# Kernel optimization log

Measured on AMD Instinct MI355X. Metric: run time of the kernel, lower is better.

## Reference

```python
import jax, jax.numpy as jnp
import numpy as np

B, S, H, NH, HD, FF, E, K = 2, 1024, 1024, 16, 64, 4096, 8, 2
EPS = 1e-6
ROPE_BASE = 10000.0


def setup_inputs() -> dict:
    key = jax.random.key(0)
    ks = jax.random.split(key, 10)
    std = 0.02
    return {
        "hidden_states": jax.random.normal(ks[0], (B, S, H), jnp.float32),
        "attention_mask": jnp.zeros((1, 1, S, S), jnp.float32),
        "ln1_w": jnp.ones((H,), jnp.float32),
        "ln2_w": jnp.ones((H,), jnp.float32),
        "Wq": jax.random.normal(ks[1], (H, H), jnp.float32) * std,
        "Wk": jax.random.normal(ks[2], (H, H), jnp.float32) * std,
        "Wv": jax.random.normal(ks[3], (H, H), jnp.float32) * std,
        "Wo": jax.random.normal(ks[4], (H, H), jnp.float32) * std,
        "Wr": jax.random.normal(ks[5], (E, H), jnp.float32) * std,
        "Wg": jax.random.normal(ks[6], (E, FF, H), jnp.float32) * std,
        "Wu": jax.random.normal(ks[7], (E, FF, H), jnp.float32) * std,
        "Wd": jax.random.normal(ks[8], (E, H, FF), jnp.float32) * std,
    }


def _rmsnorm(x, w):
    rms = jnp.sqrt(jnp.mean(x * x, axis=-1, keepdims=True) + EPS)
    return x / rms * w


def _rotate_half(x):
    x1, x2 = x[..., : x.shape[-1] // 2], x[..., x.shape[-1] // 2:]
    return jnp.concatenate((-x2, x1), axis=-1)


def _forward(hidden_states, attention_mask, ln1_w, ln2_w, Wq, Wk, Wv, Wo, Wr, Wg, Wu, Wd):
    residual = hidden_states
    x = _rmsnorm(hidden_states, ln1_w)

    # attention projections -> [B, NH, S, HD]
    def split_heads(t):
        return t.reshape(B, S, NH, HD).transpose(0, 2, 1, 3)

    q = split_heads(x @ Wq.T)
    k = split_heads(x @ Wk.T)
    v = split_heads(x @ Wv.T)

    # RoPE
    inv_freq = 1.0 / (ROPE_BASE ** (jnp.arange(0, HD, 2, dtype=jnp.float32) / HD))
    freqs = jnp.outer(jnp.arange(S, dtype=jnp.float32), inv_freq)  # [S, HD/2]
    emb = jnp.concatenate((freqs, freqs), axis=-1)  # [S, HD]
    cos = jnp.cos(emb)[None, None]
    sin = jnp.sin(emb)[None, None]
    q = q * cos + _rotate_half(q) * sin
    k = k * cos + _rotate_half(k) * sin

    scale = HD ** -0.5
    scores = jnp.einsum("bhqd,bhkd->bhqk", q, k) * scale + attention_mask
    attn = jax.nn.softmax(scores.astype(jnp.float32), axis=-1).astype(q.dtype)
    out = jnp.einsum("bhqk,bhkd->bhqd", attn, v)
    out = out.transpose(0, 2, 1, 3).reshape(B, S, H) @ Wo.T

    hidden = residual + out  # dropout is identity in eval

    # MoE FFN
    residual2 = hidden
    x2 = _rmsnorm(hidden, ln2_w)
    router_logits = x2 @ Wr.T  # [B, S, E]
    router_probs = jax.nn.softmax(router_logits, axis=-1)
    expert_weights, expert_indices = jax.lax.top_k(router_probs, K)  # [B,S,K]
    expert_weights = expert_weights / jnp.sum(expert_weights, axis=-1, keepdims=True)

    # load-balance loss
    num_tokens = B * S
    counts = jnp.sum(expert_indices[..., None] == jnp.arange(E), axis=(0, 1, 2)).astype(jnp.float32)
    expert_usage = counts / num_tokens  # [E]
    mean_routing_prob = router_probs.mean(axis=(0, 1))  # [E]
    lb_loss = jnp.sum(expert_usage * mean_routing_prob) * E

    moe_out = jnp.zeros_like(x2)
    for e in range(E):
        # combine weight is 0 for tokens not routed to expert e -> same math as masked gather/scatter
        w_e = jnp.sum(expert_weights * (expert_indices == e), axis=-1, keepdims=True)  # [B,S,1]
        y = (jax.nn.silu(x2 @ Wg[e].T) * (x2 @ Wu[e].T)) @ Wd[e].T
        moe_out = moe_out + w_e * y

    hidden = residual2 + moe_out
    return hidden, lb_loss


def reference(hidden_states, attention_mask, ln1_w, ln2_w, Wq, Wk, Wv, Wo, Wr, Wg, Wu, Wd):
    return _forward(hidden_states, attention_mask, ln1_w, ln2_w, Wq, Wk, Wv, Wo, Wr, Wg, Wu, Wd)
```

## Files before the change

### kernel.cpp

```cpp
#include <hip/hip_runtime.h>
#include <cstdint>
#include <cstddef>

#define DI __device__ __forceinline__

namespace {

constexpr int B_ = 2, S_ = 1024, H_ = 1024, NH_ = 16, FF_ = 4096, E_ = 8;
constexpr int T_ = B_ * S_;
constexpr int MAXTILES = (T_ * 2) / 128 + E_;
constexpr int PADSLOTS = MAXTILES * 128;
constexpr size_t APL = (size_t)T_ * H_;
constexpr size_t WPL = (size_t)H_ * H_;

typedef __attribute__((ext_vector_type(8))) short short8;
typedef __attribute__((ext_vector_type(4))) float f32x4;

DI float bf2f(unsigned short u) { return __uint_as_float(((unsigned)u) << 16); }
DI unsigned short f2bf(float f) {
  unsigned u = __float_as_uint(f);
  u += 0x7fffu + ((u >> 16) & 1u);
  return (unsigned short)(u >> 16);
}
DI void cvt8(const float4 a, const float4 b, unsigned short* d) {
  d[0] = f2bf(a.x); d[1] = f2bf(a.y); d[2] = f2bf(a.z); d[3] = f2bf(a.w);
  d[4] = f2bf(b.x); d[5] = f2bf(b.y); d[6] = f2bf(b.z); d[7] = f2bf(b.w);
}

template <int MODE>
__global__ __launch_bounds__(256) void rmsnorm_kernel(const float* __restrict__ in,
                                                      const float* __restrict__ w,
                                                      float* __restrict__ out,
                                                      unsigned short* __restrict__ outb) {
  const int t = blockIdx.x, tid = threadIdx.x;
  const float4* row = (const float4*)(in + (size_t)t * H_);
  float4 v = row[tid];
  float ss = v.x * v.x + v.y * v.y + v.z * v.z + v.w * v.w;
  #pragma unroll
  for (int off = 32; off; off >>= 1) ss += __shfl_down(ss, off);
  __shared__ float red[4];
  if ((tid & 63) == 0) red[tid >> 6] = ss;
  __syncthreads();
  const float total = red[0] + red[1] + red[2] + red[3];
  const float rinv = 1.f / sqrtf(total * (1.f / (float)H_) + 1e-6f);
  const float4 wv = ((const float4*)w)[tid];
  float o[4];
  o[0] = v.x * rinv * wv.x; o[1] = v.y * rinv * wv.y;
  o[2] = v.z * rinv * wv.z; o[3] = v.w * rinv * wv.w;
  if (MODE == 1) {
    float4 o4 = {o[0], o[1], o[2], o[3]};
    ((float4*)(out + (size_t)t * H_))[tid] = o4;
    unsigned short* p = outb + (size_t)t * H_ + tid * 4;
    p[0] = f2bf(o[0]); p[1] = f2bf(o[1]); p[2] = f2bf(o[2]); p[3] = f2bf(o[3]);
  } else {
    __align__(8) unsigned short hi[4], lo[4];
    #pragma unroll
    for (int j = 0; j < 4; j++) {
      hi[j] = f2bf(o[j]);
      lo[j] = f2bf(o[j] - bf2f(hi[j]));
    }
    const size_t idx = (size_t)t * H_ + tid * 4;
    *(uint2*)&outb[idx] = *(const uint2*)hi;
    *(uint2*)&outb[APL + idx] = *(const uint2*)lo;
  }
}

__global__ __launch_bounds__(256) void cvt_wsplit(const float* __restrict__ src,
                                                  unsigned short* __restrict__ dst, int n8) {
  const int i = blockIdx.x * 256 + threadIdx.x;
  if (i < n8) {
    const float4 a = ((const float4*)src)[2 * i];
    const float4 b = ((const float4*)src)[2 * i + 1];
    const float xs[8] = {a.x, a.y, a.z, a.w, b.x, b.y, b.z, b.w};
    __align__(16) unsigned short hi[8], lo[8];
    #pragma unroll
    for (int j = 0; j < 8; j++) {
      hi[j] = f2bf(xs[j]);
      lo[j] = f2bf(xs[j] - bf2f(hi[j]));
    }
    ((uint4*)dst)[i] = *(const uint4*)hi;
    ((uint4*)(dst + WPL))[i] = *(const uint4*)lo;
  }
}

__global__ __launch_bounds__(256) void cvt_ws(const float* __restrict__ src,
                                              unsigned short* __restrict__ dst, int n8) {
  const int i = blockIdx.x * 256 + threadIdx.x;
  if (i < n8) {
    const float4 a = ((const float4*)src)[2 * i];
    const float4 b = ((const float4*)src)[2 * i + 1];
    __align__(16) unsigned short t[8];
    cvt8(a, b, t);
    ((uint4*)dst)[i] = *(const uint4*)t;
  }
}

template <int EPI>
__global__ __launch_bounds__(256, 3) void gemm_split(const unsigned short* __restrict__ As,
                                                     const unsigned short* __restrict__ Wsa,
                                                     const unsigned short* __restrict__ Wsb,
                                                     const unsigned short* __restrict__ Wsc,
                                                     float* __restrict__ Ca,
                                                     float* __restrict__ Cb,
                                                     float* __restrict__ Cc,
                                                     const float* __restrict__ resid) {
  constexpr int K = 1024;
  constexpr int LDA = 40;
  __shared__ __align__(16) unsigned short sAh[128 * LDA];
  __shared__ __align__(16) unsigned short sAl[128 * LDA];
  __shared__ __align__(16) unsigned short sWh[128 * LDA];
  __shared__ __align__(16) unsigned short sWl[128 * LDA];
  const int tid = threadIdx.x;
  const int m0 = blockIdx.x << 7, n0 = blockIdx.y << 7;
  const unsigned short* W = Wsa; float* C = Ca;
  if (EPI == 0) {
    if (blockIdx.z == 1) { W = Wsb; C = Cb; }
    else if (blockIdx.z == 2) { W = Wsc; C = Cc; }
  }
  const int wave = tid >> 6, lane = tid & 63, wm = wave >> 1, wn = wave & 1;
  const int g16 = lane >> 4, l15 = lane & 15;
  const int row = tid >> 1, kq = (tid & 1) << 4;
  const unsigned short* pah = As + (size_t)(m0 + row) * K + kq;
  const unsigned short* pal = pah + APL;
  const unsigned short* pwh = W + (size_t)(n0 + row) * K + kq;
  const unsigned short* pwl = pwh + WPL;
  f32x4 acc[4][4];
  #pragma unroll
  for (int m = 0; m < 4; m++)
    #pragma unroll
    for (int n = 0; n < 4; n++) acc[m][n] = (f32x4){0.f, 0.f, 0.f, 0.f};

  uint4 rah0 = *(const uint4*)pah, rah1 = *(const uint4*)(pah + 8);
  uint4 ral0 = *(const uint4*)pal, ral1 = *(const uint4*)(pal + 8);
  uint4 rwh0 = *(const uint4*)pwh, rwh1 = *(const uint4*)(pwh + 8);
  uint4 rwl0 = *(const uint4*)pwl, rwl1 = *(const uint4*)(pwl + 8);

  for (int k0 = 0; k0 < K; k0 += 32) {
    __syncthreads();
    *(uint4*)&sAh[row * LDA + kq] = rah0;
    *(uint4*)&sAh[row * LDA + kq + 8] = rah1;
    *(uint4*)&sAl[row * LDA + kq] = ral0;
    *(uint4*)&sAl[row * LDA + kq + 8] = ral1;
    *(uint4*)&sWh[row * LDA + kq] = rwh0;
    *(uint4*)&sWh[row * LDA + kq + 8] = rwh1;
    *(uint4*)&sWl[row * LDA + kq] = rwl0;
    *(uint4*)&sWl[row * LDA + kq + 8] = rwl1;
    if (k0 + 32 < K) {
      rah0 = *(const uint4*)(pah + k0 + 32); rah1 = *(const uint4*)(pah + k0 + 40);
      ral0 = *(const uint4*)(pal + k0 + 32); ral1 = *(const uint4*)(pal + k0 + 40);
      rwh0 = *(const uint4*)(pwh + k0 + 32); rwh1 = *(const uint4*)(pwh + k0 + 40);
      rwl0 = *(const uint4*)(pwl + k0 + 32); rwl1 = *(const uint4*)(pwl + k0 + 40);
    }
    __syncthreads();
    short8 ah[4], al[4], wh[4], wl[4];
    #pragma unroll
    for (int m = 0; m < 4; m++) {
      ah[m] = *(const short8*)&sAh[(wm * 64 + m * 16 + l15) * LDA + g16 * 8];
      al[m] = *(const short8*)&sAl[(wm * 64 + m * 16 + l15) * LDA + g16 * 8];
    }
    #pragma unroll
    for (int n = 0; n < 4; n++) {
      wh[n] = *(const short8*)&sWh[(wn * 64 + n * 16 + l15) * LDA + g16 * 8];
      wl[n] = *(const short8*)&sWl[(wn * 64 + n * 16 + l15) * LDA + g16 * 8];
    }
    #pragma unroll
    for (int m = 0; m < 4; m++)
      #pragma unroll
      for (int n = 0; n < 4; n++) {
        acc[m][n] = __builtin_amdgcn_mfma_f32_16x16x32_bf16(ah[m], wh[n], acc[m][n], 0, 0, 0);
        acc[m][n] = __builtin_amdgcn_mfma_f32_16x16x32_bf16(al[m], wh[n], acc[m][n], 0, 0, 0);
        acc[m][n] = __builtin_amdgcn_mfma_f32_16x16x32_bf16(ah[m], wl[n], acc[m][n], 0, 0, 0);
      }
  }
  #pragma unroll
  for (int m = 0; m < 4; m++)
    #pragma unroll
    for (int r = 0; r < 4; r++) {
      const int grow = m0 + wm * 64 + m * 16 + g16 * 4 + r;
      #pragma unroll
      for (int n = 0; n < 4; n++) {
        const int gcol = n0 + wn * 64 + n * 16 + l15;
        float v = acc[m][n][r];
        if (EPI == 1) v += resid[(size_t)grow * 1024 + gcol];
        C[(size_t)grow * 1024 + gcol] = v;
      }
    }
}

__global__ __launch_bounds__(256) void rope_kernel(float* __restrict__ buf) {
  const int id = blockIdx.x * 256 + threadIdx.x;
  const int t = id >> 9;
  const int rem = id & 511;
  const int h = rem >> 5, j = rem & 31;
  const int s = t & (S_ - 1);
  const float inv = exp2f(-(float)j * (0.41524101186092029f));
  const float ang = (float)s * inv;
  const float c = cosf(ang), sn = sinf(ang);
  float* p = buf + (size_t)t * H_ + h * 64;
  const float xa = p[j], xb = p[j + 32];
  p[j] = xa * c - xb * sn;
  p[j + 32] = xb * c + xa * sn;
}

__global__ __launch_bounds__(512, 2) void attn_mfma(const float* __restrict__ q,
                                                    const float* __restrict__ k,
                                                    const float* __restrict__ v,
                                                    unsigned short* __restrict__ aos) {
  constexpr int LDW = 136;
  __shared__ __align__(16) unsigned short sP[128 * LDW];
  __shared__ __align__(16) unsigned short sK[64 * LDW];
  __shared__ __align__(16) unsigned short sVt[64 * LDW];
  const int tid = threadIdx.x;
  const int bh = blockIdx.x >> 3, chunk = blockIdx.x & 7;
  const int b = bh >> 4, h = bh & (NH_ - 1);
  const int w = tid >> 6, lane = tid & 63, g = lane >> 4, l15 = lane & 15;

  {
    const int row = tid >> 2, d0 = (tid & 3) << 4;
    const float* qp = q + ((size_t)((b << 10) + (chunk << 7) + row)) * H_ + h * 64 + d0;
    __align__(16) unsigned short thi[16], tlo[16];
    #pragma unroll
    for (int c = 0; c < 4; c++) {
      const float4 x = ((const float4*)qp)[c];
      const float xs[4] = {x.x, x.y, x.z, x.w};
      #pragma unroll
      for (int j = 0; j < 4; j++) {
        const float val = xs[j] * 0.125f;
        const unsigned short hi = f2bf(val);
        thi[c * 4 + j] = hi;
        tlo[c * 4 + j] = f2bf(val - bf2f(hi));
      }
    }
    uint4* dh = (uint4*)&sP[row * LDW + d0];
    dh[0] = ((const uint4*)thi)[0]; dh[1] = ((const uint4*)thi)[1];
    uint4* dl = (uint4*)&sP[row * LDW + 64 + d0];
    dl[0] = ((const uint4*)tlo)[0]; dl[1] = ((const uint4*)tlo)[1];
  }
  __syncthreads();
  short8 aqh[2], aql[2];
  #pragma unroll
  for (int s2 = 0; s2 < 2; s2++) {
    aqh[s2] = *(const short8*)&sP[(w * 16 + l15) * LDW + s2 * 32 + g * 8];
    aql[s2] = *(const short8*)&sP[(w * 16 + l15) * LDW + 64 + s2 * 32 + g * 8];
  }
  __syncthreads();

  f32x4 accO[4];
  #pragma unroll
  for (int n = 0; n < 4; n++) accO[n] = (f32x4){0.f, 0.f, 0.f, 0.f};
  float mrun[4] = {-3.0e38f, -3.0e38f, -3.0e38f, -3.0e38f};
  float lrun[4] = {0.f, 0.f, 0.f, 0.f};

  const int krow = tid >> 3, dk0 = (tid & 7) << 3;
  const int vd = tid >> 3, vk0 = (tid & 7) << 3;
  const float* kp0 = k + ((size_t)((b << 10) + krow)) * H_ + h * 64 + dk0;
  const float* vp0 = v + ((size_t)(b << 10)) * H_ + h * 64 + vd;

  float krg[8], vrg[8];
  {
    const float4 a = *(const float4*)kp0;
    const float4 c = *(const float4*)(kp0 + 4);
    krg[0] = a.x; krg[1] = a.y; krg[2] = a.z; krg[3] = a.w;
    krg[4] = c.x; krg[5] = c.y; krg[6] = c.z; krg[7] = c.w;
    #pragma unroll
    for (int i = 0; i < 8; i++) vrg[i] = vp0[(size_t)(vk0 + i) * H_];
  }
  {
    __align__(16) unsigned short thi[8], tlo[8];
    #pragma unroll
    for (int j = 0; j < 8; j++) {
      const unsigned short hi = f2bf(krg[j]);
      thi[j] = hi; tlo[j] = f2bf(krg[j] - bf2f(hi));
    }
    *(uint4*)&sK[krow * LDW + dk0] = *(const uint4*)thi;
    *(uint4*)&sK[krow * LDW + 64 + dk0] = *(const uint4*)tlo;
    #pragma unroll
    for (int j = 0; j < 8; j++) {
      const unsigned short hi = f2bf(vrg[j]);
      thi[j] = hi; tlo[j] = f2bf(vrg[j] - bf2f(hi));
    }
    *(uint4*)&sVt[vd * LDW + vk0] = *(const uint4*)thi;
    *(uint4*)&sVt[vd * LDW + 64 + vk0] = *(const uint4*)tlo;
  }
  __syncthreads();

  for (int kt = 0; kt < S_ / 64; kt++) {
    if (kt < S_ / 64 - 1) {
      const float* kp = kp0 + (size_t)((kt + 1) * 64) * H_;
      const float4 a = *(const float4*)kp;
      const float4 c = *(const float4*)(kp + 4);
      krg[0] = a.x; krg[1] = a.y; krg[2] = a.z; krg[3] = a.w;
      krg[4] = c.x; krg[5] = c.y; krg[6] = c.z; krg[7] = c.w;
      #pragma unroll
      for (int i = 0; i < 8; i++) vrg[i] = vp0[(size_t)((kt + 1) * 64 + vk0 + i) * H_];
    }
    f32x4 accS[4];
    #pragma unroll
    for (int n = 0; n < 4; n++) accS[n] = (f32x4){0.f, 0.f, 0.f, 0.f};
    #pragma unroll
    for (int s2 = 0; s2 < 2; s2++) {
      #pragma unroll
      for (int n = 0; n < 4; n++) {
        const short8 bkh = *(const short8*)&sK[(n * 16 + l15) * LDW + s2 * 32 + g * 8];
        const short8 bkl = *(const short8*)&sK[(n * 16 + l15) * LDW + 64 + s2 * 32 + g * 8];
        accS[n] = __builtin_amdgcn_mfma_f32_16x16x32_bf16(aqh[s2], bkh, accS[n], 0, 0, 0);
        accS[n] = __builtin_amdgcn_mfma_f32_16x16x32_bf16(aql[s2], bkh, accS[n], 0, 0, 0);
        accS[n] = __builtin_amdgcn_mfma_f32_16x16x32_bf16(aqh[s2], bkl, accS[n], 0, 0, 0);
      }
    }
    float corr[4];
    float pv_[4][4];
    #pragma unroll
    for (int r = 0; r < 4; r++) {
      float tm = fmaxf(fmaxf(accS[0][r], accS[1][r]), fmaxf(accS[2][r], accS[3][r]));
      tm = fmaxf(tm, __shfl_xor(tm, 1));
      tm = fmaxf(tm, __shfl_xor(tm, 2));
      tm = fmaxf(tm, __shfl_xor(tm, 4));
      tm = fmaxf(tm, __shfl_xor(tm, 8));
      const float mnew = fmaxf(mrun[r], tm);
      corr[r] = __expf(mrun[r] - mnew);
      mrun[r] = mnew;
      float ssum = 0.f;
      #pragma unroll
      for (int n = 0; n < 4; n++) {
        const float p = __expf(accS[n][r] - mnew);
        pv_[n][r] = p; ssum += p;
      }
      ssum += __shfl_xor(ssum, 1);
      ssum += __shfl_xor(ssum, 2);
      ssum += __shfl_xor(ssum, 4);
      ssum += __shfl_xor(ssum, 8);
      lrun[r] = lrun[r] * corr[r] + ssum;
    }
    #pragma unroll
    for (int n = 0; n < 4; n++)
      #pragma unroll
      for (int r = 0; r < 4; r++) accO[n][r] *= corr[r];
    #pragma unroll
    for (int n = 0; n < 4; n++)
      #pragma unroll
      for (int r = 0; r < 4; r++) {
        const float p = pv_[n][r];
        const unsigned short hi = f2bf(p);
        unsigned short* pp = &sP[(w * 16 + g * 4 + r) * LDW + (n * 16 + l15)];
        pp[0] = hi;
        pp[64] = f2bf(p - bf2f(hi));
      }
    #pragma unroll
    for (int s2 = 0; s2 < 2; s2++) {
      const short8 aph = *(const short8*)&sP[(w * 16 + l15) * LDW + s2 * 32 + g * 8];
      const short8 apl = *(const short8*)&sP[(w * 16 + l15) * LDW + 64 + s2 * 32 + g * 8];
      #pragma unroll
      for (int n = 0; n < 4; n++) {
        const short8 bvh = *(const short8*)&sVt[(n * 16 + l15) * LDW + s2 * 32 + g * 8];
        const short8 bvl = *(const short8*)&sVt[(n * 16 + l15) * LDW + 64 + s2 * 32 + g * 8];
        accO[n] = __builtin_amdgcn_mfma_f32_16x16x32_bf16(aph, bvh, accO[n], 0, 0, 0);
        accO[n] = __builtin_amdgcn_mfma_f32_16x16x32_bf16(apl, bvh, accO[n], 0, 0, 0);
        accO[n] = __builtin_amdgcn_mfma_f32_16x16x32_bf16(aph, bvl, accO[n], 0, 0, 0);
      }
    }
    __syncthreads();
    if (kt < S_ / 64 - 1) {
      __align__(16) unsigned short thi[8], tlo[8];
      #pragma unroll
      for (int j = 0; j < 8; j++) {
        const unsigned short hi = f2bf(krg[j]);
        thi[j] = hi; tlo[j] = f2bf(krg[j] - bf2f(hi));
      }
      *(uint4*)&sK[krow * LDW + dk0] = *(const uint4*)thi;
      *(uint4*)&sK[krow * LDW + 64 + dk0] = *(const uint4*)tlo;
      #pragma unroll
      for (int j = 0; j < 8; j++) {
        const unsigned short hi = f2bf(vrg[j]);
        thi[j] = hi; tlo[j] = f2bf(vrg[j] - bf2f(hi));
      }
      *(uint4*)&sVt[vd * LDW + vk0] = *(const uint4*)thi;
      *(uint4*)&sVt[vd * LDW + 64 + vk0] = *(const uint4*)tlo;
    }
    __syncthreads();
  }
  float inv[4];
  #pragma unroll
  for (int r = 0; r < 4; r++) inv[r] = 1.f / lrun[r];
  unsigned short* aoh = aos + ((size_t)((b << 10) + (chunk << 7) + w * 16)) * H_ + h * 64;
  #pragma unroll
  for (int n = 0; n < 4; n++)
    #pragma unroll
    for (int r = 0; r < 4; r++) {
      const float val = accO[n][r] * inv[r];
      const unsigned short hi = f2bf(val);
      const size_t idx = (size_t)(g * 4 + r) * H_ + n * 16 + l15;
      aoh[idx] = hi;
      aoh[APL + idx] = f2bf(val - bf2f(hi));
    }
}

__global__ __launch_bounds__(256) void router_kernel(const float* __restrict__ x2,
                                                     const float* __restrict__ Wr,
                                                     float* __restrict__ probs,
                                                     int* __restrict__ texp,
                                                     float* __restrict__ tw) {
  const int wid = threadIdx.x >> 6, lane = threadIdx.x & 63;
  const int t = (blockIdx.x << 2) + wid;
  const float* xr = x2 + (size_t)t * H_;
  float4 xv[4];
  #pragma unroll
  for (int i = 0; i < 4; i++) xv[i] = *(const float4*)&xr[(i << 8) + (lane << 2)];
  float acc[E_];
  #pragma unroll
  for (int e = 0; e < E_; e++) acc[e] = 0.f;
  #pragma unroll
  for (int i = 0; i < 4; i++) {
    #pragma unroll
    for (int e = 0; e < E_; e++) {
      const float4 wv = *(const float4*)&Wr[e * H_ + (i << 8) + (lane << 2)];
      acc[e] += xv[i].x * wv.x + xv[i].y * wv.y + xv[i].z * wv.z + xv[i].w * wv.w;
    }
  }
  #pragma unroll
  for (int e = 0; e < E_; e++) {
    #pragma unroll
    for (int off = 32; off; off >>= 1) acc[e] += __shfl_xor(acc[e], off);
  }
  if (lane == 0) {
    float mx = acc[0];
    #pragma unroll
    for (int e = 1; e < E_; e++) mx = fmaxf(mx, acc[e]);
    float pp[E_]; float sum = 0.f;
    #pragma unroll
    for (int e = 0; e < E_; e++) { pp[e] = __expf(acc[e] - mx); sum += pp[e]; }
    const float isum = 1.f / sum;
    #pragma unroll
    for (int e = 0; e < E_; e++) pp[e] *= isum;
    float4 p0 = {pp[0], pp[1], pp[2], pp[3]};
    float4 p1 = {pp[4], pp[5], pp[6], pp[7]};
    *(float4*)&probs[(size_t)t * E_] = p0;
    *(float4*)&probs[(size_t)t * E_ + 4] = p1;
    int e0 = 0; float b0 = pp[0];
    #pragma unroll
    for (int e = 1; e < E_; e++) if (pp[e] > b0) { b0 = pp[e]; e0 = e; }
    int e1 = -1; float b1 = -1.f;
    #pragma unroll
    for (int e = 0; e < E_; e++) if (e != e0 && pp[e] > b1) { b1 = pp[e]; e1 = e; }
    const float iw = 1.f / (b0 + b1);
    texp[2 * t] = e0; texp[2 * t + 1] = e1;
    tw[2 * t] = b0 * iw; tw[2 * t + 1] = b1 * iw;
  }
}

__global__ __launch_bounds__(256) void fill_slots(int* slot_tok, float* slot_w) {
  const int i = blockIdx.x * 256 + threadIdx.x;
  if (i < PADSLOTS) { slot_tok[i] = -1; slot_w[i] = 0.f; }
}

__global__ __launch_bounds__(256) void finalize_kernel(const float* __restrict__ probs,
                                                       const int* __restrict__ texp,
                                                       const float* __restrict__ tw,
                                                       int* __restrict__ ntiles,
                                                       int* __restrict__ tile_expert,
                                                       int* __restrict__ slot_tok,
                                                       float* __restrict__ slot_w,
                                                       float* __restrict__ lb_out) {
  const int tid = threadIdx.x;
  const int w = tid >> 6, lane = tid & 63;
  __shared__ float sRed[4][E_];
  __shared__ int sCnt[4][E_];
  __shared__ int sPoff[E_];
  __shared__ int sBase[E_];
  __shared__ int sWcnt[4][E_];

  float ps[E_];
  #pragma unroll
  for (int e = 0; e < E_; e++) ps[e] = 0.f;
  #pragma unroll
  for (int i = 0; i < T_ / 256; i++) {
    const float4* pr = (const float4*)&probs[(size_t)(i * 256 + tid) * E_];
    const float4 a = pr[0], b = pr[1];
    ps[0] += a.x; ps[1] += a.y; ps[2] += a.z; ps[3] += a.w;
    ps[4] += b.x; ps[5] += b.y; ps[6] += b.z; ps[7] += b.w;
  }
  #pragma unroll
  for (int e = 0; e < E_; e++) {
    #pragma unroll
    for (int off = 32; off; off >>= 1) ps[e] += __shfl_xor(ps[e], off);
  }
  int cnt[E_];
  #pragma unroll
  for (int e = 0; e < E_; e++) cnt[e] = 0;
  #pragma unroll
  for (int i = 0; i < 2 * T_ / 256; i++) {
    const int ee = texp[i * 256 + tid];
    #pragma unroll
    for (int e = 0; e < E_; e++) cnt[e] += (ee == e) ? 1 : 0;
  }
  #pragma unroll
  for (int e = 0; e < E_; e++) {
    #pragma unroll
    for (int off = 32; off; off >>= 1) cnt[e] += __shfl_xor(cnt[e], off);
  }
  if (lane == 0) {
    #pragma unroll
    for (int e = 0; e < E_; e++) { sRed[w][e] = ps[e]; sCnt[w][e] = cnt[e]; }
  }
  __syncthreads();
  if (tid == 0) {
    int off = 0, tc = 0;
    float lb = 0.f;
    for (int e = 0; e < E_; e++) {
      const int c = sCnt[0][e] + sCnt[1][e] + sCnt[2][e] + sCnt[3][e];
      const float p = sRed[0][e] + sRed[1][e] + sRed[2][e] + sRed[3][e];
      sPoff[e] = off;
      const int nt = (c + 127) >> 7;
      for (int i = 0; i < nt; i++) tile_expert[tc++] = e;
      off += nt << 7;
      lb += ((float)c / (float)T_) * (p / (float)T_);
    }
    *ntiles = tc;
    lb_out[0] = lb * (float)E_;
  }
  if (tid < E_) sBase[tid] = 0;
  __syncthreads();
  for (int c = 0; c < 2 * T_ / 256; c++) {
    const int i = c * 256 + tid;
    const int e = texp[i];
    const float wv = tw[i];
    int myrank = 0;
    #pragma unroll
    for (int ee = 0; ee < E_; ee++) {
      const unsigned long long m = __ballot(e == ee);
      if (lane == 0) sWcnt[w][ee] = (int)__popcll(m);
      if (e == ee) myrank = (int)__popcll(m & ((1ull << lane) - 1ull));
    }
    __syncthreads();
    int pre = 0;
    #pragma unroll
    for (int w2 = 0; w2 < 4; w2++) if (w2 < w) pre += sWcnt[w2][e];
    const int slot = sPoff[e] + sBase[e] + pre + myrank;
    slot_tok[slot] = i >> 1;
    slot_w[slot] = wv;
    __syncthreads();
    if (tid < E_) sBase[tid] += sWcnt[0][tid] + sWcnt[1][tid] + sWcnt[2][tid] + sWcnt[3][tid];
    __syncthreads();
  }
}

__global__ __launch_bounds__(256, 2) void moe_gemm1(const unsigned short* __restrict__ x2b,
                                                    const float* __restrict__ Wg,
                                                    const float* __restrict__ Wu,
                                                    const int* __restrict__ slot_tok,
                                                    const int* __restrict__ tile_expert,
                                                    const int* __restrict__ ntiles,
                                                    unsigned short* __restrict__ hbuf) {
  const int bid = blockIdx.x;
  const int tile = bid >> 6;
  const int n0 = (bid & 63) << 6;
  if (tile >= *ntiles) return;
  constexpr int K = 1024;
  constexpr int LDA = 72;
  __shared__ __align__(16) unsigned short sA[128 * LDA];
  __shared__ __align__(16) unsigned short sG[64 * LDA];
  __shared__ __align__(16) unsigned short sU[64 * LDA];
  __shared__ int stok[128];
  const int tid = threadIdx.x;
  if (tid < 128) stok[tid] = slot_tok[tile * 128 + tid];
  __syncthreads();
  const int e = tile_expert[tile];
  const int wave = tid >> 6, lane = tid & 63, wm = wave >> 1, wn = wave & 1;
  const int g16 = lane >> 4, l15 = lane & 15;
  const int arow = tid >> 2, akq = (tid & 3) << 4;
  const int grow = tid >> 2, gkq = (tid & 3) << 3;
  int tok0 = stok[arow];       if (tok0 < 0) tok0 = 0;
  int tok1 = stok[64 + arow];  if (tok1 < 0) tok1 = 0;
  const unsigned short* a0 = x2b + (size_t)tok0 * K + akq;
  const unsigned short* a1 = x2b + (size_t)tok1 * K + akq;
  const float* gp = Wg + ((size_t)e * FF_ + n0 + grow) * K + gkq;
  const float* up = Wu + ((size_t)e * FF_ + n0 + grow) * K + gkq;

  f32x4 ag[4][2], au[4][2];
  #pragma unroll
  for (int m = 0; m < 4; m++)
    #pragma unroll
    for (int n = 0; n < 2; n++) { ag[m][n] = (f32x4){0,0,0,0}; au[m][n] = (f32x4){0,0,0,0}; }

  uint4 ra0 = *(const uint4*)a0, ra1 = *(const uint4*)(a0 + 8);
  uint4 ra2 = *(const uint4*)a1, ra3 = *(const uint4*)(a1 + 8);
  float4 rg[4], ru[4];
  rg[0] = *(const float4*)gp;        rg[1] = *(const float4*)(gp + 4);
  rg[2] = *(const float4*)(gp + 32); rg[3] = *(const float4*)(gp + 36);
  ru[0] = *(const float4*)up;        ru[1] = *(const float4*)(up + 4);
  ru[2] = *(const float4*)(up + 32); ru[3] = *(const float4*)(up + 36);

  for (int k0 = 0; k0 < K; k0 += 64) {
    __align__(16) unsigned short tg[16], tu[16];
    cvt8(rg[0], rg[1], tg); cvt8(rg[2], rg[3], tg + 8);
    cvt8(ru[0], ru[1], tu); cvt8(ru[2], ru[3], tu + 8);
    __syncthreads();
    *(uint4*)&sA[arow * LDA + akq] = ra0;
    *(uint4*)&sA[arow * LDA + akq + 8] = ra1;
    *(uint4*)&sA[(arow + 64) * LDA + akq] = ra2;
    *(uint4*)&sA[(arow + 64) * LDA + akq + 8] = ra3;
    *(uint4*)&sG[grow * LDA + gkq] = ((const uint4*)tg)[0];
    *(uint4*)&sG[grow * LDA + gkq + 32] = ((const uint4*)tg)[1];
    *(uint4*)&sU[grow * LDA + gkq] = ((const uint4*)tu)[0];
    *(uint4*)&sU[grow * LDA + gkq + 32] = ((const uint4*)tu)[1];
    if (k0 + 64 < K) {
      ra0 = *(const uint4*)(a0 + k0 + 64); ra1 = *(const uint4*)(a0 + k0 + 72);
      ra2 = *(const uint4*)(a1 + k0 + 64); ra3 = *(const uint4*)(a1 + k0 + 72);
      rg[0] = *(const float4*)(gp + k0 + 64); rg[1] = *(const float4*)(gp + k0 + 68);
      rg[2] = *(const float4*)(gp + k0 + 96); rg[3] = *(const float4*)(gp + k0 + 100);
      ru[0] = *(const float4*)(up + k0 + 64); ru[1] = *(const float4*)(up + k0 + 68);
      ru[2] = *(const float4*)(up + k0 + 96); ru[3] = *(const float4*)(up + k0 + 100);
    }
    __syncthreads();
    #pragma unroll
    for (int ks = 0; ks < 2; ks++) {
      const int ko = ks * 32 + g16 * 8;
      short8 af[4], gf[2], uf[2];
      #pragma unroll
      for (int m = 0; m < 4; m++)
        af[m] = *(const short8*)&sA[(wm * 64 + m * 16 + l15) * LDA + ko];
      #pragma unroll
      for (int n = 0; n < 2; n++) {
        gf[n] = *(const short8*)&sG[(wn * 32 + n * 16 + l15) * LDA + ko];
        uf[n] = *(const short8*)&sU[(wn * 32 + n * 16 + l15) * LDA + ko];
      }
      #pragma unroll
      for (int m = 0; m < 4; m++)
        #pragma unroll
        for (int n = 0; n < 2; n++) {
          ag[m][n] = __builtin_amdgcn_mfma_f32_16x16x32_bf16(af[m], gf[n], ag[m][n], 0, 0, 0);
          au[m][n] = __builtin_amdgcn_mfma_f32_16x16x32_bf16(af[m], uf[n], au[m][n], 0, 0, 0);
        }
    }
  }
  #pragma unroll
  for (int m = 0; m < 4; m++)
    #pragma unroll
    for (int r = 0; r < 4; r++) {
      const int slotloc = wm * 64 + m * 16 + g16 * 4 + r;
      unsigned short* hr = hbuf + (size_t)(tile * 128 + slotloc) * FF_ + n0;
      #pragma unroll
      for (int n = 0; n < 2; n++) {
        const int col = wn * 32 + n * 16 + l15;
        const float g = ag[m][n][r], u = au[m][n][r];
        const float hv = (g / (1.f + __expf(-g))) * u;
        hr[col] = f2bf(hv);
      }
    }
}

__global__ __launch_bounds__(256, 2) void moe_gemm2(const unsigned short* __restrict__ hbuf,
                                                    const unsigned short* __restrict__ Wdb,
                                                    const int* __restrict__ slot_tok,
                                                    const float* __restrict__ slot_w,
                                                    const int* __restrict__ tile_expert,
                                                    const int* __restrict__ ntiles,
                                                    float* __restrict__ out) {
  const int bid = blockIdx.x;
  const int tile = bid % MAXTILES;
  const int n0 = (bid / MAXTILES) << 7;
  if (tile >= *ntiles) return;
  constexpr int K = 4096;
  constexpr int LDA = 72;
  __shared__ __align__(16) unsigned short sA[128 * LDA];
  __shared__ __align__(16) unsigned short sB[128 * LDA];
  __shared__ int s_tok[128];
  __shared__ float s_w[128];
  const int tid = threadIdx.x;
  if (tid < 128) { s_tok[tid] = slot_tok[tile * 128 + tid]; s_w[tid] = slot_w[tile * 128 + tid]; }
  const int e = tile_expert[tile];
  const int wave = tid >> 6, lane = tid & 63, wm = wave >> 1, wn = wave & 1;
  const int g16 = lane >> 4, l15 = lane & 15;
  const int arow = tid >> 1, akq = (tid & 1) << 4;
  const unsigned short* ap = hbuf + (size_t)(tile * 128 + arow) * K + akq;
  const unsigned short* wp = Wdb + ((size_t)e * H_ + n0 + arow) * K + akq;

  f32x4 acc[4][4];
  #pragma unroll
  for (int m = 0; m < 4; m++)
    #pragma unroll
    for (int n = 0; n < 4; n++) acc[m][n] = (f32x4){0,0,0,0};

  uint4 ra0 = *(const uint4*)ap, ra1 = *(const uint4*)(ap + 8);
  uint4 ra2 = *(const uint4*)(ap + 32), ra3 = *(const uint4*)(ap + 40);
  uint4 rb0 = *(const uint4*)wp, rb1 = *(const uint4*)(wp + 8);
  uint4 rb2 = *(const uint4*)(wp + 32), rb3 = *(const uint4*)(wp + 40);

  for (int k0 = 0; k0 < K; k0 += 64) {
    __syncthreads();
    *(uint4*)&sA[arow * LDA + akq] = ra0;
    *(uint4*)&sA[arow * LDA + akq + 8] = ra1;
    *(uint4*)&sA[arow * LDA + akq + 32] = ra2;
    *(uint4*)&sA[arow * LDA + akq + 40] = ra3;
    *(uint4*)&sB[arow * LDA + akq] = rb0;
    *(uint4*)&sB[arow * LDA + akq + 8] = rb1;
    *(uint4*)&sB[arow * LDA + akq + 32] = rb2;
    *(uint4*)&sB[arow * LDA + akq + 40] = rb3;
    if (k0 + 64 < K) {
      ra0 = *(const uint4*)(ap + k0 + 64); ra1 = *(const uint4*)(ap + k0 + 72);
      ra2 = *(const uint4*)(ap + k0 + 96); ra3 = *(const uint4*)(ap + k0 + 104);
      rb0 = *(const uint4*)(wp + k0 + 64); rb1 = *(const uint4*)(wp + k0 + 72);
      rb2 = *(const uint4*)(wp + k0 + 96); rb3 = *(const uint4*)(wp + k0 + 104);
    }
    __syncthreads();
    #pragma unroll
    for (int ks = 0; ks < 2; ks++) {
      const int ko = ks * 32 + g16 * 8;
      short8 af[4], bf_[4];
      #pragma unroll
      for (int m = 0; m < 4; m++)
        af[m] = *(const short8*)&sA[(wm * 64 + m * 16 + l15) * LDA + ko];
      #pragma unroll
      for (int n = 0; n < 4; n++)
        bf_[n] = *(const short8*)&sB[(wn * 64 + n * 16 + l15) * LDA + ko];
      #pragma unroll
      for (int m = 0; m < 4; m++)
        #pragma unroll
        for (int n = 0; n < 4; n++)
          acc[m][n] = __builtin_amdgcn_mfma_f32_16x16x32_bf16(af[m], bf_[n], acc[m][n], 0, 0, 0);
    }
  }
  #pragma unroll
  for (int m = 0; m < 4; m++)
    #pragma unroll
    for (int r = 0; r < 4; r++) {
      const int slotloc = wm * 64 + m * 16 + g16 * 4 + r;
      const int tok = s_tok[slotloc];
      if (tok < 0) continue;
      const float wv = s_w[slotloc];
      float* orow = out + (size_t)tok * H_ + n0;
      #pragma unroll
      for (int n = 0; n < 4; n++) {
        const int col = wn * 64 + n * 16 + l15;
        atomicAdd(&orow[col], wv * acc[m][n][r]);
      }
    }
}

}

extern "C" void kernel_launch(void* const* d_in, const int* in_sizes, int n_in,
                              void* d_out, int out_size, void* d_ws, size_t ws_size,
                              hipStream_t stream) {
  const float* hs  = (const float*)d_in[0];
  const float* ln1 = (const float*)d_in[2];
  const float* ln2 = (const float*)d_in[3];
  const float* Wq  = (const float*)d_in[4];
  const float* Wk  = (const float*)d_in[5];
  const float* Wv  = (const float*)d_in[6];
  const float* Wo  = (const float*)d_in[7];
  const float* Wr  = (const float*)d_in[8];
  const float* Wg  = (const float*)d_in[9];
  const float* Wu  = (const float*)d_in[10];
  const float* Wd  = (const float*)d_in[11];
  float* out = (float*)d_out;
  char* ws = (char*)d_ws;

  constexpr size_t MB = (size_t)1 << 20;
  unsigned short* x1s = (unsigned short*)(ws);
  float* qb  = (float*)(ws + 8 * MB);
  float* kb  = (float*)(ws + 16 * MB);
  float* vb  = (float*)(ws + 24 * MB);
  unsigned short* aos = (unsigned short*)(ws + 32 * MB);
  float* x2  = (float*)(ws + 40 * MB);
  unsigned short* x2b  = (unsigned short*)(ws + 48 * MB);
  unsigned short* hbuf = (unsigned short*)(ws + 52 * MB);
  unsigned short* wqs = (unsigned short*)(ws + 52 * MB);
  unsigned short* wks = (unsigned short*)(ws + 56 * MB);
  unsigned short* wvs = (unsigned short*)(ws + 60 * MB);
  unsigned short* wos = (unsigned short*)(ws + 64 * MB);
  char* meta = ws + 92 * MB;
  int*   ntl     = (int*)(meta + 256);
  int*   texpert = (int*)(meta + 512);
  int*   texp    = (int*)(meta + 1024);
  float* tw      = (float*)(meta + 1024 + 16384);
  int*   stok    = (int*)(meta + 1024 + 32768);
  float* sw      = (float*)(meta + 1024 + 32768 + (size_t)PADSLOTS * 4);
  float* probs   = (float*)(meta + 1024 + 32768 + (size_t)PADSLOTS * 8);
  constexpr size_t WELEMS = (size_t)E_ * FF_ * H_;
  unsigned short* wdb = (unsigned short*)(ws + 96 * MB);

  const int wblk = (int)(WPL / 8 / 256);
  cvt_wsplit<<<dim3(wblk), 256, 0, stream>>>(Wq, wqs, (int)(WPL / 8));
  cvt_wsplit<<<dim3(wblk), 256, 0, stream>>>(Wk, wks, (int)(WPL / 8));
  cvt_wsplit<<<dim3(wblk), 256, 0, stream>>>(Wv, wvs, (int)(WPL / 8));
  cvt_wsplit<<<dim3(wblk), 256, 0, stream>>>(Wo, wos, (int)(WPL / 8));

  rmsnorm_kernel<2><<<dim3(T_), dim3(256), 0, stream>>>(hs, ln1, nullptr, x1s);

  gemm_split<0><<<dim3(16, 8, 3), 256, 0, stream>>>(x1s, wqs, wks, wvs, qb, kb, vb, nullptr);

  const int rope_blocks = (T_ * NH_ * 32) / 256;
  rope_kernel<<<dim3(rope_blocks), 256, 0, stream>>>(qb);
  rope_kernel<<<dim3(rope_blocks), 256, 0, stream>>>(kb);

  attn_mfma<<<dim3(B_ * NH_ * (S_ / 128)), 512, 0, stream>>>(qb, kb, vb, aos);

  gemm_split<1><<<dim3(16, 8, 1), 256, 0, stream>>>(aos, wos, nullptr, nullptr, out, nullptr, nullptr, hs);

  rmsnorm_kernel<1><<<dim3(T_), dim3(256), 0, stream>>>(out, ln2, x2, x2b);
  router_kernel<<<dim3(T_ / 4), 256, 0, stream>>>(x2, Wr, probs, texp, tw);
  fill_slots<<<dim3(PADSLOTS / 256), 256, 0, stream>>>(stok, sw);
  finalize_kernel<<<dim3(1), dim3(256), 0, stream>>>(probs, texp, tw, ntl, texpert,
                                                     stok, sw, out + (size_t)T_ * H_);

  moe_gemm1<<<dim3(MAXTILES * (FF_ / 64)), 256, 0, stream>>>(x2b, Wg, Wu, stok, texpert, ntl, hbuf);

  const int cvt_blocks = (int)(WELEMS / 8 / 256);
  cvt_ws<<<dim3(cvt_blocks), 256, 0, stream>>>(Wd, wdb, (int)(WELEMS / 8));

  moe_gemm2<<<dim3(MAXTILES * (H_ / 128)), 256, 0, stream>>>(hbuf, wdb, stok, sw, texpert, ntl, out);
}
```

Before: 469.4 us.

## Fuse RoPE, Q scaling and bf16 hi/lo split into QKV GEMM epilogue

The QKV projection epilogue now applies RoPE to Q and K, folds the 1/sqrt(d) scale into Q, and writes split bf16 hi/lo planes directly, removing the two separate rope kernels. The attention kernel then loads pre-split bf16 Q/K/V instead of converting fp32 on every tile load. This removes the fp32 intermediate round trips, two launches and repeated conversion work inside attention. The cost is transcendental work in the GEMM epilogue and scattered 2-byte stores there.

```diff
diff --git a/kernel.cpp b/kernel.cpp
--- a/kernel.cpp
+++ b/kernel.cpp
@@ -100,9 +100,10 @@
                                                      const unsigned short* __restrict__ Wsa,
                                                      const unsigned short* __restrict__ Wsb,
                                                      const unsigned short* __restrict__ Wsc,
-                                                     float* __restrict__ Ca,
-                                                     float* __restrict__ Cb,
-                                                     float* __restrict__ Cc,
+                                                     unsigned short* __restrict__ Csa,
+                                                     unsigned short* __restrict__ Csb,
+                                                     unsigned short* __restrict__ Csc,
+                                                     float* __restrict__ Cf,
                                                      const float* __restrict__ resid) {
   constexpr int K = 1024;
   constexpr int LDA = 40;
@@ -112,10 +113,11 @@
   __shared__ __align__(16) unsigned short sWl[128 * LDA];
   const int tid = threadIdx.x;
   const int m0 = blockIdx.x << 7, n0 = blockIdx.y << 7;
-  const unsigned short* W = Wsa; float* C = Ca;
+  const unsigned short* W = Wsa;
+  unsigned short* Cs = Csa;
   if (EPI == 0) {
-    if (blockIdx.z == 1) { W = Wsb; C = Cb; }
-    else if (blockIdx.z == 2) { W = Wsc; C = Cc; }
+    if (blockIdx.z == 1) { W = Wsb; Cs = Csb; }
+    else if (blockIdx.z == 2) { W = Wsc; Cs = Csc; }
   }
   const int wave = tid >> 6, lane = tid & 63, wm = wave >> 1, wn = wave & 1;
   const int g16 = lane >> 4, l15 = lane & 15;
@@ -172,39 +174,59 @@
         acc[m][n] = __builtin_amdgcn_mfma_f32_16x16x32_bf16(ah[m], wl[n], acc[m][n], 0, 0, 0);
       }
   }
-  #pragma unroll
-  for (int m = 0; m < 4; m++)
-    #pragma unroll
-    for (int r = 0; r < 4; r++) {
-      const int grow = m0 + wm * 64 + m * 16 + g16 * 4 + r;
-      #pragma unroll
-      for (int n = 0; n < 4; n++) {
-        const int gcol = n0 + wn * 64 + n * 16 + l15;
-        float v = acc[m][n][r];
-        if (EPI == 1) v += resid[(size_t)grow * 1024 + gcol];
-        C[(size_t)grow * 1024 + gcol] = v;
-      }
-    }
-}
-
-__global__ __launch_bounds__(256) void rope_kernel(float* __restrict__ buf) {
-  const int id = blockIdx.x * 256 + threadIdx.x;
-  const int t = id >> 9;
-  const int rem = id & 511;
-  const int h = rem >> 5, j = rem & 31;
-  const int s = t & (S_ - 1);
-  const float inv = exp2f(-(float)j * (0.41524101186092029f));
-  const float ang = (float)s * inv;
-  const float c = cosf(ang), sn = sinf(ang);
-  float* p = buf + (size_t)t * H_ + h * 64;
-  const float xa = p[j], xb = p[j + 32];
-  p[j] = xa * c - xb * sn;
-  p[j + 32] = xb * c + xa * sn;
-}
-
-__global__ __launch_bounds__(512, 2) void attn_mfma(const float* __restrict__ q,
-                                                    const float* __restrict__ k,
-                                                    const float* __restrict__ v,
+  if (EPI == 1) {
+    #pragma unroll
+    for (int m = 0; m < 4; m++)
+      #pragma unroll
+      for (int r = 0; r < 4; r++) {
+        const int grow = m0 + wm * 64 + m * 16 + g16 * 4 + r;
+        #pragma unroll
+        for (int n = 0; n < 4; n++) {
+          const int gcol = n0 + wn * 64 + n * 16 + l15;
+          Cf[(size_t)grow * 1024 + gcol] = acc[m][n][r] + resid[(size_t)grow * 1024 + gcol];
+        }
+      }
+  } else {
+    const bool isQ = (blockIdx.z == 0);
+    const bool isV = (blockIdx.z == 2);
+    #pragma unroll
+    for (int m = 0; m < 4; m++)
+      #pragma unroll
+      for (int r = 0; r < 4; r++) {
+        const int t = m0 + wm * 64 + m * 16 + g16 * 4 + r;
+        const int s = t & (S_ - 1);
+        #pragma unroll
+        for (int n = 0; n < 2; n++) {
+          const int j = n * 16 + l15;
+          const int gcol = n0 + wn * 64 + j;
+          const float xa = acc[m][n][r];
+          const float xb = acc[m][n + 2][r];
+          float lowv, highv;
+          if (!isV) {
+            const float inv = exp2f(-(float)j * (0.41524101186092029f));
+            const float ang = (float)s * inv;
+            const float c = cosf(ang), sn = sinf(ang);
+            lowv = xa * c - xb * sn;
+            highv = xb * c + xa * sn;
+            if (isQ) { lowv *= 0.125f; highv *= 0.125f; }
+          } else {
+            lowv = xa; highv = xb;
+          }
+          const unsigned short h1 = f2bf(lowv);
+          const unsigned short h2 = f2bf(highv);
+          const size_t i1 = (size_t)t * 1024 + gcol;
+          Cs[i1] = h1;
+          Cs[APL + i1] = f2bf(lowv - bf2f(h1));
+          Cs[i1 + 32] = h2;
+          Cs[APL + i1 + 32] = f2bf(highv - bf2f(h2));
+        }
+      }
+  }
+}
+
+__global__ __launch_bounds__(512, 2) void attn_mfma(const unsigned short* __restrict__ qs,
+                                                    const unsigned short* __restrict__ ks,
+                                                    const unsigned short* __restrict__ vs,
                                                     unsigned short* __restrict__ aos) {
   constexpr int LDW = 136;
   __shared__ __align__(16) unsigned short sP[128 * LDW];
@@ -217,24 +239,11 @@
 
   {
     const int row = tid >> 2, d0 = (tid & 3) << 4;
-    const float* qp = q + ((size_t)((b << 10) + (chunk << 7) + row)) * H_ + h * 64 + d0;
-    __align__(16) unsigned short thi[16], tlo[16];
-    #pragma unroll
-    for (int c = 0; c < 4; c++) {
-      const float4 x = ((const float4*)qp)[c];
-      const float xs[4] = {x.x, x.y, x.z, x.w};
-      #pragma unroll
-      for (int j = 0; j < 4; j++) {
-        const float val = xs[j] * 0.125f;
-        const unsigned short hi = f2bf(val);
-        thi[c * 4 + j] = hi;
-        tlo[c * 4 + j] = f2bf(val - bf2f(hi));
-      }
-    }
-    uint4* dh = (uint4*)&sP[row * LDW + d0];
-    dh[0] = ((const uint4*)thi)[0]; dh[1] = ((const uint4*)thi)[1];
-    uint4* dl = (uint4*)&sP[row * LDW + 64 + d0];
-    dl[0] = ((const uint4*)tlo)[0]; dl[1] = ((const uint4*)tlo)[1];
+    const unsigned short* qp = qs + ((size_t)((b << 10) + (chunk << 7) + row)) * H_ + h * 64 + d0;
+    *(uint4*)&sP[row * LDW + d0] = *(const uint4*)qp;
+    *(uint4*)&sP[row * LDW + d0 + 8] = *(const uint4*)(qp + 8);
+    *(uint4*)&sP[row * LDW + 64 + d0] = *(const uint4*)(qp + APL);
+    *(uint4*)&sP[row * LDW + 64 + d0 + 8] = *(const uint4*)(qp + APL + 8);
   }
   __syncthreads();
   short8 aqh[2], aql[2];
@@ -253,46 +262,36 @@
 
   const int krow = tid >> 3, dk0 = (tid & 7) << 3;
   const int vd = tid >> 3, vk0 = (tid & 7) << 3;
-  const float* kp0 = k + ((size_t)((b << 10) + krow)) * H_ + h * 64 + dk0;
-  const float* vp0 = v + ((size_t)(b << 10)) * H_ + h * 64 + vd;
-
-  float krg[8], vrg[8];
+  const unsigned short* kp0 = ks + ((size_t)((b << 10) + krow)) * H_ + h * 64 + dk0;
+  const unsigned short* vp0 = vs + ((size_t)(b << 10)) * H_ + h * 64 + vd;
+
+  uint4 khr, klr;
+  __align__(16) unsigned short vhr[8], vlr[8];
   {
-    const float4 a = *(const float4*)kp0;
-    const float4 c = *(const float4*)(kp0 + 4);
-    krg[0] = a.x; krg[1] = a.y; krg[2] = a.z; krg[3] = a.w;
-    krg[4] = c.x; krg[5] = c.y; krg[6] = c.z; krg[7] = c.w;
-    #pragma unroll
-    for (int i = 0; i < 8; i++) vrg[i] = vp0[(size_t)(vk0 + i) * H_];
-  }
-  {
-    __align__(16) unsigned short thi[8], tlo[8];
-    #pragma unroll
-    for (int j = 0; j < 8; j++) {
-      const unsigned short hi = f2bf(krg[j]);
-      thi[j] = hi; tlo[j] = f2bf(krg[j] - bf2f(hi));
-    }
-    *(uint4*)&sK[krow * LDW + dk0] = *(const uint4*)thi;
-    *(uint4*)&sK[krow * LDW + 64 + dk0] = *(const uint4*)tlo;
-    #pragma unroll
-    for (int j = 0; j < 8; j++) {
-      const unsigned short hi = f2bf(vrg[j]);
-      thi[j] = hi; tlo[j] = f2bf(vrg[j] - bf2f(hi));
-    }
-    *(uint4*)&sVt[vd * LDW + vk0] = *(const uint4*)thi;
-    *(uint4*)&sVt[vd * LDW + 64 + vk0] = *(const uint4*)tlo;
-  }
+    khr = *(const uint4*)kp0;
+    klr = *(const uint4*)(kp0 + APL);
+    #pragma unroll
+    for (int i = 0; i < 8; i++) {
+      vhr[i] = vp0[(size_t)(vk0 + i) * H_];
+      vlr[i] = vp0[APL + (size_t)(vk0 + i) * H_];
+    }
+  }
+  *(uint4*)&sK[krow * LDW + dk0] = khr;
+  *(uint4*)&sK[krow * LDW + 64 + dk0] = klr;
+  *(uint4*)&sVt[vd * LDW + vk0] = *(const uint4*)vhr;
+  *(uint4*)&sVt[vd * LDW + 64 + vk0] = *(const uint4*)vlr;
   __syncthreads();
 
   for (int kt = 0; kt < S_ / 64; kt++) {
     if (kt < S_ / 64 - 1) {
-      const float* kp = kp0 + (size_t)((kt + 1) * 64) * H_;
-      const float4 a = *(const float4*)kp;
-      const float4 c = *(const float4*)(kp + 4);
-      krg[0] = a.x; krg[1] = a.y; krg[2] = a.z; krg[3] = a.w;
-      krg[4] = c.x; krg[5] = c.y; krg[6] = c.z; krg[7] = c.w;
-      #pragma unroll
-      for (int i = 0; i < 8; i++) vrg[i] = vp0[(size_t)((kt + 1) * 64 + vk0 + i) * H_];
+      const unsigned short* kp = kp0 + (size_t)((kt + 1) * 64) * H_;
+      khr = *(const uint4*)kp;
+      klr = *(const uint4*)(kp + APL);
+      #pragma unroll
+      for (int i = 0; i < 8; i++) {
+        vhr[i] = vp0[(size_t)((kt + 1) * 64 + vk0 + i) * H_];
+        vlr[i] = vp0[APL + (size_t)((kt + 1) * 64 + vk0 + i) * H_];
+      }
     }
     f32x4 accS[4];
     #pragma unroll
@@ -361,21 +360,10 @@
     }
     __syncthreads();
     if (kt < S_ / 64 - 1) {
-      __align__(16) unsigned short thi[8], tlo[8];
-      #pragma unroll
-      for (int j = 0; j < 8; j++) {
-        const unsigned short hi = f2bf(krg[j]);
-        thi[j] = hi; tlo[j] = f2bf(krg[j] - bf2f(hi));
-      }
-      *(uint4*)&sK[krow * LDW + dk0] = *(const uint4*)thi;
-      *(uint4*)&sK[krow * LDW + 64 + dk0] = *(const uint4*)tlo;
-      #pragma unroll
-      for (int j = 0; j < 8; j++) {
-        const unsigned short hi = f2bf(vrg[j]);
-        thi[j] = hi; tlo[j] = f2bf(vrg[j] - bf2f(hi));
-      }
-      *(uint4*)&sVt[vd * LDW + vk0] = *(const uint4*)thi;
-      *(uint4*)&sVt[vd * LDW + 64 + vk0] = *(const uint4*)tlo;
+      *(uint4*)&sK[krow * LDW + dk0] = khr;
+      *(uint4*)&sK[krow * LDW + 64 + dk0] = klr;
+      *(uint4*)&sVt[vd * LDW + vk0] = *(const uint4*)vhr;
+      *(uint4*)&sVt[vd * LDW + 64 + vk0] = *(const uint4*)vlr;
     }
     __syncthreads();
   }
@@ -758,9 +746,9 @@
 
   constexpr size_t MB = (size_t)1 << 20;
   unsigned short* x1s = (unsigned short*)(ws);
-  float* qb  = (float*)(ws + 8 * MB);
-  float* kb  = (float*)(ws + 16 * MB);
-  float* vb  = (float*)(ws + 24 * MB);
+  unsigned short* qs  = (unsigned short*)(ws + 8 * MB);
+  unsigned short* ks  = (unsigned short*)(ws + 16 * MB);
+  unsigned short* vs  = (unsigned short*)(ws + 24 * MB);
   unsigned short* aos = (unsigned short*)(ws + 32 * MB);
   float* x2  = (float*)(ws + 40 * MB);
   unsigned short* x2b  = (unsigned short*)(ws + 48 * MB);
@@ -788,15 +776,13 @@
 
   rmsnorm_kernel<2><<<dim3(T_), dim3(256), 0, stream>>>(hs, ln1, nullptr, x1s);
 
-  gemm_split<0><<<dim3(16, 8, 3), 256, 0, stream>>>(x1s, wqs, wks, wvs, qb, kb, vb, nullptr);
-
-  const int rope_blocks = (T_ * NH_ * 32) / 256;
-  rope_kernel<<<dim3(rope_blocks), 256, 0, stream>>>(qb);
-  rope_kernel<<<dim3(rope_blocks), 256, 0, stream>>>(kb);
-
-  attn_mfma<<<dim3(B_ * NH_ * (S_ / 128)), 512, 0, stream>>>(qb, kb, vb, aos);
-
-  gemm_split<1><<<dim3(16, 8, 1), 256, 0, stream>>>(aos, wos, nullptr, nullptr, out, nullptr, nullptr, hs);
+  gemm_split<0><<<dim3(16, 8, 3), 256, 0, stream>>>(x1s, wqs, wks, wvs,
+                                                    qs, ks, vs, nullptr, nullptr);
+
+  attn_mfma<<<dim3(B_ * NH_ * (S_ / 128)), 512, 0, stream>>>(qs, ks, vs, aos);
+
+  gemm_split<1><<<dim3(16, 8, 1), 256, 0, stream>>>(aos, wos, nullptr, nullptr,
+                                                    nullptr, nullptr, nullptr, out, hs);
 
   rmsnorm_kernel<1><<<dim3(T_), dim3(256), 0, stream>>>(out, ln2, x2, x2b);
   router_kernel<<<dim3(T_ / 4), 256, 0, stream>>>(x2, Wr, probs, texp, tw);
```

Result: no change. 476.5 us (+1.5%).
